# Performance work log

Measured on AMD Instinct MI355X. Metric: run time of the kernel, lower is better.

Reference implementation:

```python
import jax, jax.numpy as jnp
import numpy as np

S, B, I, H, O = 256, 128, 512, 1024, 32


def _lstm_layer(x, w_ih, w_hh, b_ih, b_hh):
    # x: [S, B, Din]; PyTorch gate order: i, f, g, o
    xg = jnp.einsum('sbi,gi->sbg', x, w_ih) + b_ih + b_hh  # [S, B, 4H] precomputed input gates
    Hd = w_hh.shape[1]

    def step(carry, xt):
        h, c = carry
        g = xt + h @ w_hh.T  # [B, 4H]
        i, f, gg, o = jnp.split(g, 4, axis=-1)
        c = jax.nn.sigmoid(f) * c + jax.nn.sigmoid(i) * jnp.tanh(gg)
        h = jax.nn.sigmoid(o) * jnp.tanh(c)
        return (h, c), h

    h0 = jnp.zeros((x.shape[1], Hd), x.dtype)
    (_, _), hs = jax.lax.scan(step, (h0, h0), xg)
    return hs  # [S, B, H]


def setup_inputs() -> dict:
    key = jax.random.key(0)
    ks = jax.random.split(key, 12)
    bound = 1.0 / np.sqrt(H)
    u = lambda k, shape: jax.random.uniform(k, shape, jnp.float32, -bound, bound)
    return {
        'input': jax.random.normal(ks[0], (S, B, I), jnp.float32),
        'w_ih_l0': u(ks[1], (4 * H, I)),
        'w_hh_l0': u(ks[2], (4 * H, H)),
        'b_ih_l0': u(ks[3], (4 * H,)),
        'b_hh_l0': u(ks[4], (4 * H,)),
        'w_ih_l1': u(ks[5], (4 * H, H)),
        'w_hh_l1': u(ks[6], (4 * H, H)),
        'b_ih_l1': u(ks[7], (4 * H,)),
        'b_hh_l1': u(ks[8], (4 * H,)),
        'w_out': u(ks[9], (O, H)),
        'b_out': u(ks[10], (O,)),
    }


def reference(input, w_ih_l0, w_hh_l0, b_ih_l0, b_hh_l0,
              w_ih_l1, w_hh_l1, b_ih_l1, b_hh_l1, w_out, b_out):
    h1 = _lstm_layer(input, w_ih_l0, w_hh_l0, b_ih_l0, b_hh_l0)  # layer 0
    h2 = _lstm_layer(h1, w_ih_l1, w_hh_l1, b_ih_l1, b_hh_l1)    # layer 1
    # original: self.h2o(hidden[4]) -> linear head on timestep index 4
    return h2[4] @ w_out.T + b_out  # [B, O]
```

## Files before the change

kernel.cpp:

```cpp
#include <hip/hip_runtime.h>
#include <hip/hip_bf16.h>
#include <math.h>

#define B_SZ 128
#define I_DIM 512
#define H_DIM 1024
#define O_DIM 32
#define G4 4096
#define NSTEP 5

using short8 = __attribute__((ext_vector_type(8))) short;
using f32x4  = __attribute__((ext_vector_type(4))) float;

__device__ inline unsigned short f2bf(float f) {
    unsigned int u = __float_as_uint(f);
    return (unsigned short)((u + 0x7fffu + ((u >> 16) & 1u)) >> 16);
}
__device__ inline float bf2f(unsigned short h) {
    return __uint_as_float(((unsigned int)h) << 16);
}
__device__ inline float sigf(float x) { return 1.f / (1.f + expf(-x)); }

#define MFMA3(ACC, AH, AL, BH, BL)                                           \
    ACC = __builtin_amdgcn_mfma_f32_16x16x32_bf16(AH, BH, ACC, 0, 0, 0);     \
    ACC = __builtin_amdgcn_mfma_f32_16x16x32_bf16(AH, BL, ACC, 0, 0, 0);     \
    ACC = __builtin_amdgcn_mfma_f32_16x16x32_bf16(AL, BH, ACC, 0, 0, 0);

__global__ __launch_bounds__(256) void init_misc(
    float* __restrict__ c0, float* __restrict__ c1,
    unsigned short* __restrict__ h0hi, unsigned short* __restrict__ h0lo,
    unsigned short* __restrict__ h1hi, unsigned short* __restrict__ h1lo,
    const float* __restrict__ bih0, const float* __restrict__ bhh0,
    const float* __restrict__ bih1, const float* __restrict__ bhh1,
    float* __restrict__ bsum0, float* __restrict__ bsum1)
{
    int i = blockIdx.x * 256 + threadIdx.x;
    if (i < B_SZ * H_DIM) {
        c0[i] = 0.f; c1[i] = 0.f;
        h0hi[i] = 0; h0lo[i] = 0; h1hi[i] = 0; h1lo[i] = 0;
    }
    if (i < G4) {
        bsum0[i] = bih0[i] + bhh0[i];
        bsum1[i] = bih1[i] + bhh1[i];
    }
}

__global__ __launch_bounds__(256) void conv_split(
    const float* __restrict__ s0, const float* __restrict__ s1,
    const float* __restrict__ s2, const float* __restrict__ s3,
    const float* __restrict__ s4,
    unsigned short* __restrict__ h0, unsigned short* __restrict__ l0,
    unsigned short* __restrict__ h1, unsigned short* __restrict__ l1,
    unsigned short* __restrict__ h2, unsigned short* __restrict__ l2,
    unsigned short* __restrict__ h3, unsigned short* __restrict__ l3,
    unsigned short* __restrict__ h4, unsigned short* __restrict__ l4)
{
    const long long E0 = 2097152;
    const long long E1 = E0 + 4194304;
    const long long E2 = E1 + 4194304;
    const long long E3 = E2 + 4194304;
    const long long E4 = E3 + 327680;
    long long i4 = ((long long)blockIdx.x * 256 + threadIdx.x) * 4;
    if (i4 >= E4) return;
    const float* s; unsigned short *hh, *ll; long long base;
    if      (i4 < E0) { s = s0; hh = h0; ll = l0; base = 0;  }
    else if (i4 < E1) { s = s1; hh = h1; ll = l1; base = E0; }
    else if (i4 < E2) { s = s2; hh = h2; ll = l2; base = E1; }
    else if (i4 < E3) { s = s3; hh = h3; ll = l3; base = E2; }
    else              { s = s4; hh = h4; ll = l4; base = E3; }
    long long k = i4 - base;
    float4 v = *(const float4*)(s + k);
    ushort4 hv, lv;
    hv.x = f2bf(v.x); lv.x = f2bf(v.x - bf2f(hv.x));
    hv.y = f2bf(v.y); lv.y = f2bf(v.y - bf2f(hv.y));
    hv.z = f2bf(v.z); lv.z = f2bf(v.z - bf2f(hv.z));
    hv.w = f2bf(v.w); lv.w = f2bf(v.w - bf2f(hv.w));
    *(ushort4*)(hh + k) = hv;
    *(ushort4*)(ll + k) = lv;
}

__global__ __launch_bounds__(256) void gemm_in(
    const unsigned short* __restrict__ xhi, const unsigned short* __restrict__ xlo,
    const unsigned short* __restrict__ whi, const unsigned short* __restrict__ wlo,
    const float* __restrict__ bsum, float* __restrict__ xg)
{
    const int tid = threadIdx.x, lane = tid & 63, wv = tid >> 6;
    const int r = lane & 15, g = lane >> 4;
    const int wm = (wv & 1) * 32, wn = (wv >> 1) * 32;
    const int bm = blockIdx.y * 64, bn = blockIdx.x * 64;
    f32x4 acc[2][2];
    const f32x4 z = {0.f, 0.f, 0.f, 0.f};
    acc[0][0] = z; acc[0][1] = z; acc[1][0] = z; acc[1][1] = z;

    const unsigned short* Ah = xhi + (bm + wm + r) * I_DIM + g * 8;
    const unsigned short* Al = xlo + (bm + wm + r) * I_DIM + g * 8;
    const unsigned short* Bh = whi + (bn + wn + r) * I_DIM + g * 8;
    const unsigned short* Bl = wlo + (bn + wn + r) * I_DIM + g * 8;

    #pragma unroll 4
    for (int k = 0; k < I_DIM; k += 32) {
        short8 a0h = *(const short8*)(Ah + k);
        short8 a0l = *(const short8*)(Al + k);
        short8 a1h = *(const short8*)(Ah + 16 * I_DIM + k);
        short8 a1l = *(const short8*)(Al + 16 * I_DIM + k);
        short8 b0h = *(const short8*)(Bh + k);
        short8 b0l = *(const short8*)(Bl + k);
        short8 b1h = *(const short8*)(Bh + 16 * I_DIM + k);
        short8 b1l = *(const short8*)(Bl + 16 * I_DIM + k);
        MFMA3(acc[0][0], a0h, a0l, b0h, b0l);
        MFMA3(acc[0][1], a0h, a0l, b1h, b1l);
        MFMA3(acc[1][0], a1h, a1l, b0h, b0l);
        MFMA3(acc[1][1], a1h, a1l, b1h, b1l);
    }
    #pragma unroll
    for (int mf = 0; mf < 2; ++mf)
        #pragma unroll
        for (int nf = 0; nf < 2; ++nf)
            #pragma unroll
            for (int j = 0; j < 4; ++j) {
                int row = bm + wm + mf * 16 + g * 4 + j;
                int col = bn + wn + nf * 16 + r;
                xg[row * G4 + col] = acc[mf][nf][j] + bsum[col];
            }
}

template<int LAYER>
__global__ __launch_bounds__(512) void lstm_step(
    const unsigned short* __restrict__ a1hi, const unsigned short* __restrict__ a1lo,
    const unsigned short* __restrict__ w1hi, const unsigned short* __restrict__ w1lo,
    const unsigned short* __restrict__ a2hi, const unsigned short* __restrict__ a2lo,
    const unsigned short* __restrict__ w2hi, const unsigned short* __restrict__ w2lo,
    const float* __restrict__ extra,
    float* __restrict__ cst,
    unsigned short* __restrict__ hohi, unsigned short* __restrict__ holo)
{
    __shared__ float lds_p[8][B_SZ][17];
    const int tid = threadIdx.x, lane = tid & 63, wv = tid >> 6;
    const int r = lane & 15, g = lane >> 4;
    const int jb = blockIdx.x * 4;
    const int q = r >> 2, j4 = r & 3;
    const int wrow = q * H_DIM + jb + j4;

    f32x4 acc[8];
    const f32x4 z = {0.f, 0.f, 0.f, 0.f};
    #pragma unroll
    for (int mf = 0; mf < 8; ++mf) acc[mf] = z;

    if (LAYER == 0) {
        const int kb = wv * 128;
        const unsigned short* Wh = w1hi + (long long)wrow * H_DIM + kb + g * 8;
        const unsigned short* Wl = w1lo + (long long)wrow * H_DIM + kb + g * 8;
        const unsigned short* Ah = a1hi + kb + g * 8;
        const unsigned short* Al = a1lo + kb + g * 8;
        #pragma unroll
        for (int ks = 0; ks < 4; ++ks) {
            short8 bh = *(const short8*)(Wh + ks * 32);
            short8 bl = *(const short8*)(Wl + ks * 32);
            #pragma unroll
            for (int mf = 0; mf < 8; ++mf) {
                int off = (mf * 16 + r) * H_DIM + ks * 32;
                short8 ah = *(const short8*)(Ah + off);
                short8 al = *(const short8*)(Al + off);
                MFMA3(acc[mf], ah, al, bh, bl);
            }
        }
    } else {
        const int kb = (wv & 3) * 256;
        const unsigned short* Wsrc_h = (wv < 4) ? w1hi : w2hi;
        const unsigned short* Wsrc_l = (wv < 4) ? w1lo : w2lo;
        const unsigned short* Asrc_h = (wv < 4) ? a1hi : a2hi;
        const unsigned short* Asrc_l = (wv < 4) ? a1lo : a2lo;
        const unsigned short* Wh = Wsrc_h + (long long)wrow * H_DIM + kb + g * 8;
        const unsigned short* Wl = Wsrc_l + (long long)wrow * H_DIM + kb + g * 8;
        const unsigned short* Ah = Asrc_h + kb + g * 8;
        const unsigned short* Al = Asrc_l + kb + g * 8;
        #pragma unroll
        for (int ks = 0; ks < 8; ++ks) {
            short8 bh = *(const short8*)(Wh + ks * 32);
            short8 bl = *(const short8*)(Wl + ks * 32);
            #pragma unroll
            for (int mf = 0; mf < 8; ++mf) {
                int off = (mf * 16 + r) * H_DIM + ks * 32;
                short8 ah = *(const short8*)(Ah + off);
                short8 al = *(const short8*)(Al + off);
                MFMA3(acc[mf], ah, al, bh, bl);
            }
        }
    }

    #pragma unroll
    for (int mf = 0; mf < 8; ++mf)
        #pragma unroll
        for (int j = 0; j < 4; ++j)
            lds_p[wv][mf * 16 + g * 4 + j][r] = acc[mf][j];
    __syncthreads();

    {
        int b = tid & 127, jj = tid >> 7;
        float gs[4];
        #pragma unroll
        for (int qq = 0; qq < 4; ++qq) {
            int col = qq * 4 + jj;
            float s = 0.f;
            #pragma unroll
            for (int w = 0; w < 8; ++w) s += lds_p[w][b][col];
            s += (LAYER == 0) ? extra[b * G4 + qq * H_DIM + jb + jj]
                              : extra[qq * H_DIM + jb + jj];
            gs[qq] = s;
        }
        int idx = b * H_DIM + jb + jj;
        float cn = sigf(gs[1]) * cst[idx] + sigf(gs[0]) * tanhf(gs[2]);
        cst[idx] = cn;
        float h = sigf(gs[3]) * tanhf(cn);
        unsigned short hh = f2bf(h);
        hohi[idx] = hh;
        holo[idx] = f2bf(h - bf2f(hh));
    }
}

__global__ __launch_bounds__(64) void head_kernel(
    const unsigned short* __restrict__ hhi, const unsigned short* __restrict__ hlo,
    const float* __restrict__ w_out, const float* __restrict__ b_out,
    float* __restrict__ out)
{
    int o = blockIdx.x, b = blockIdx.y, lane = threadIdx.x;
    const unsigned short* hp = hhi + b * H_DIM;
    const unsigned short* lp = hlo + b * H_DIM;
    const float* wp = w_out + o * H_DIM;
    float s = 0.f;
    #pragma unroll
    for (int k = lane; k < H_DIM; k += 64)
        s += (bf2f(hp[k]) + bf2f(lp[k])) * wp[k];
    #pragma unroll
    for (int off = 32; off; off >>= 1) s += __shfl_down(s, off);
    if (lane == 0) out[b * O_DIM + o] = s + b_out[o];
}

extern "C" void kernel_launch(void* const* d_in, const int* in_sizes, int n_in,
                              void* d_out, int out_size, void* d_ws, size_t ws_size,
                              hipStream_t stream)
{
    const float* input   = (const float*)d_in[0];
    const float* w_ih_l0 = (const float*)d_in[1];
    const float* w_hh_l0 = (const float*)d_in[2];
    const float* b_ih_l0 = (const float*)d_in[3];
    const float* b_hh_l0 = (const float*)d_in[4];
    const float* w_ih_l1 = (const float*)d_in[5];
    const float* w_hh_l1 = (const float*)d_in[6];
    const float* b_ih_l1 = (const float*)d_in[7];
    const float* b_hh_l1 = (const float*)d_in[8];
    const float* w_out   = (const float*)d_in[9];
    const float* b_out   = (const float*)d_in[10];
    float* out = (float*)d_out;

    char* base = (char*)d_ws;
    size_t off = 0;
    auto alloc = [&](size_t bytes) { char* p = base + off; off = (off + bytes + 255) & ~(size_t)255; return p; };
    unsigned short* wih0_hi = (unsigned short*)alloc(2097152 * 2);
    unsigned short* wih0_lo = (unsigned short*)alloc(2097152 * 2);
    unsigned short* whh0_hi = (unsigned short*)alloc(4194304 * 2);
    unsigned short* whh0_lo = (unsigned short*)alloc(4194304 * 2);
    unsigned short* wih1_hi = (unsigned short*)alloc(4194304 * 2);
    unsigned short* wih1_lo = (unsigned short*)alloc(4194304 * 2);
    unsigned short* whh1_hi = (unsigned short*)alloc(4194304 * 2);
    unsigned short* whh1_lo = (unsigned short*)alloc(4194304 * 2);
    unsigned short* xhi     = (unsigned short*)alloc(327680 * 2);
    unsigned short* xlo     = (unsigned short*)alloc(327680 * 2);
    float* xg0   = (float*)alloc((size_t)NSTEP * B_SZ * G4 * 4);
    float* bsum0 = (float*)alloc(G4 * 4);
    float* bsum1 = (float*)alloc(G4 * 4);
    float* c0    = (float*)alloc(B_SZ * H_DIM * 4);
    float* c1    = (float*)alloc(B_SZ * H_DIM * 4);
    unsigned short* h0hi[2], *h0lo[2], *h1hi[2], *h1lo[2];
    for (int i = 0; i < 2; ++i) {
        h0hi[i] = (unsigned short*)alloc(B_SZ * H_DIM * 2);
        h0lo[i] = (unsigned short*)alloc(B_SZ * H_DIM * 2);
        h1hi[i] = (unsigned short*)alloc(B_SZ * H_DIM * 2);
        h1lo[i] = (unsigned short*)alloc(B_SZ * H_DIM * 2);
    }

    init_misc<<<(B_SZ * H_DIM + 255) / 256, 256, 0, stream>>>(
        c0, c1, h0hi[0], h0lo[0], h1hi[0], h1lo[0],
        b_ih_l0, b_hh_l0, b_ih_l1, b_hh_l1, bsum0, bsum1);

    conv_split<<<(15007744 / 4 + 255) / 256, 256, 0, stream>>>(
        w_ih_l0, w_hh_l0, w_ih_l1, w_hh_l1, input,
        wih0_hi, wih0_lo, whh0_hi, whh0_lo, wih1_hi, wih1_lo,
        whh1_hi, whh1_lo, xhi, xlo);

    gemm_in<<<dim3(G4 / 64, (NSTEP * B_SZ) / 64), 256, 0, stream>>>(
        xhi, xlo, wih0_hi, wih0_lo, bsum0, xg0);

    for (int t = 0; t < NSTEP; ++t) {
        int in = t & 1, o2 = 1 - in;
        lstm_step<0><<<H_DIM / 4, 512, 0, stream>>>(
            h0hi[in], h0lo[in], whh0_hi, whh0_lo,
            nullptr, nullptr, nullptr, nullptr,
            xg0 + (size_t)t * B_SZ * G4, c0, h0hi[o2], h0lo[o2]);
        lstm_step<1><<<H_DIM / 4, 512, 0, stream>>>(
            h0hi[o2], h0lo[o2], wih1_hi, wih1_lo,
            h1hi[in], h1lo[in], whh1_hi, whh1_lo,
            bsum1, c1, h1hi[o2], h1lo[o2]);
    }

    head_kernel<<<dim3(O_DIM, B_SZ), 64, 0, stream>>>(
        h1hi[1], h1lo[1], w_out, b_out, out);
}
```

Baseline: 519.5 us.

## Pack bf16 weights and hidden states into MFMA fragment-tiled layout

The fp32-to-bf16 hi/lo conversion now writes weights, input and hidden states in a pre-tiled layout where each 16x32 MFMA fragment is contiguous, so every lane loads its short8 from consecutive addresses. The gemm_in, lstm_step and head kernels index this tiled layout, and the recurrent weights are grouped per output block so the gate rows a block needs sit together. The goal is fully coalesced global loads in place of strided row accesses. In exchange the conversion kernel does scattered writes, the hidden-state stores become scattered 2-byte writes, and the cell state is stored transposed.

```diff
diff --git a/kernel.cpp b/kernel.cpp
--- a/kernel.cpp
+++ b/kernel.cpp
@@ -25,6 +25,7 @@
     ACC = __builtin_amdgcn_mfma_f32_16x16x32_bf16(AH, BH, ACC, 0, 0, 0);     \
     ACC = __builtin_amdgcn_mfma_f32_16x16x32_bf16(AH, BL, ACC, 0, 0, 0);     \
     ACC = __builtin_amdgcn_mfma_f32_16x16x32_bf16(AL, BH, ACC, 0, 0, 0);
+
 
 __global__ __launch_bounds__(256) void init_misc(
     float* __restrict__ c0, float* __restrict__ c1,
@@ -45,68 +46,85 @@
     }
 }
 
-__global__ __launch_bounds__(256) void conv_split(
-    const float* __restrict__ s0, const float* __restrict__ s1,
-    const float* __restrict__ s2, const float* __restrict__ s3,
-    const float* __restrict__ s4,
-    unsigned short* __restrict__ h0, unsigned short* __restrict__ l0,
-    unsigned short* __restrict__ h1, unsigned short* __restrict__ l1,
-    unsigned short* __restrict__ h2, unsigned short* __restrict__ l2,
-    unsigned short* __restrict__ h3, unsigned short* __restrict__ l3,
-    unsigned short* __restrict__ h4, unsigned short* __restrict__ l4)
-{
-    const long long E0 = 2097152;
-    const long long E1 = E0 + 4194304;
-    const long long E2 = E1 + 4194304;
-    const long long E3 = E2 + 4194304;
-    const long long E4 = E3 + 327680;
-    long long i4 = ((long long)blockIdx.x * 256 + threadIdx.x) * 4;
-    if (i4 >= E4) return;
-    const float* s; unsigned short *hh, *ll; long long base;
-    if      (i4 < E0) { s = s0; hh = h0; ll = l0; base = 0;  }
-    else if (i4 < E1) { s = s1; hh = h1; ll = l1; base = E0; }
-    else if (i4 < E2) { s = s2; hh = h2; ll = l2; base = E1; }
-    else if (i4 < E3) { s = s3; hh = h3; ll = l3; base = E2; }
-    else              { s = s4; hh = h4; ll = l4; base = E3; }
-    long long k = i4 - base;
-    float4 v = *(const float4*)(s + k);
-    ushort4 hv, lv;
-    hv.x = f2bf(v.x); lv.x = f2bf(v.x - bf2f(hv.x));
-    hv.y = f2bf(v.y); lv.y = f2bf(v.y - bf2f(hv.y));
-    hv.z = f2bf(v.z); lv.z = f2bf(v.z - bf2f(hv.z));
-    hv.w = f2bf(v.w); lv.w = f2bf(v.w - bf2f(hv.w));
-    *(ushort4*)(hh + k) = hv;
-    *(ushort4*)(ll + k) = lv;
+__global__ __launch_bounds__(256) void conv_pack(
+    const float* __restrict__ s_wih0, const float* __restrict__ s_whh0,
+    const float* __restrict__ s_wih1, const float* __restrict__ s_whh1,
+    const float* __restrict__ s_x,
+    unsigned short* __restrict__ d_wih0h, unsigned short* __restrict__ d_wih0l,
+    unsigned short* __restrict__ d_whh0h, unsigned short* __restrict__ d_whh0l,
+    unsigned short* __restrict__ d_wih1h, unsigned short* __restrict__ d_wih1l,
+    unsigned short* __restrict__ d_whh1h, unsigned short* __restrict__ d_whh1l,
+    unsigned short* __restrict__ d_xh,   unsigned short* __restrict__ d_xl)
+{
+    const long long G0 = 262144;
+    const long long G1 = G0 + 524288;
+    const long long G2 = G1 + 524288;
+    const long long G3 = G2 + 524288;
+    const long long GT = G3 + 40960;
+    long long i8 = (long long)blockIdx.x * 256 + threadIdx.x;
+    if (i8 >= GT) return;
+    const float* src; unsigned short *dh, *dl;
+    int row, k8, K, blockpk;
+    if (i8 < G0)      { long long lg = i8;      src = s_wih0; dh = d_wih0h; dl = d_wih0l; K = 512;  blockpk = 0; row = (int)(lg >> 6);  k8 = (int)(lg & 63);  }
+    else if (i8 < G1) { long long lg = i8 - G0; src = s_whh0; dh = d_whh0h; dl = d_whh0l; K = 1024; blockpk = 1; row = (int)(lg >> 7);  k8 = (int)(lg & 127); }
+    else if (i8 < G2) { long long lg = i8 - G1; src = s_wih1; dh = d_wih1h; dl = d_wih1l; K = 1024; blockpk = 1; row = (int)(lg >> 7);  k8 = (int)(lg & 127); }
+    else if (i8 < G3) { long long lg = i8 - G2; src = s_whh1; dh = d_whh1h; dl = d_whh1l; K = 1024; blockpk = 1; row = (int)(lg >> 7);  k8 = (int)(lg & 127); }
+    else              { long long lg = i8 - G3; src = s_x;    dh = d_xh;    dl = d_xl;    K = 512;  blockpk = 0; row = (int)(lg >> 6);  k8 = (int)(lg & 63);  }
+    int kt = k8 >> 2, g = k8 & 3;
+    long long dst;
+    if (blockpk) {
+        int j = row & 1023, q = row >> 10;
+        int r = q * 4 + (j & 3);
+        dst = (((long long)(j >> 2) * 32 + kt) * 64 + g * 16 + r) * 8;
+    } else {
+        int NKT = K >> 5;
+        dst = (((long long)(row >> 4) * NKT + kt) * 64 + g * 16 + (row & 15)) * 8;
+    }
+    const float* p = src + (long long)row * K + k8 * 8;
+    float4 a = *(const float4*)p;
+    float4 b = *(const float4*)(p + 4);
+    float v[8] = {a.x, a.y, a.z, a.w, b.x, b.y, b.z, b.w};
+    short8 hv, lv;
+    #pragma unroll
+    for (int i = 0; i < 8; ++i) {
+        unsigned short h = f2bf(v[i]);
+        hv[i] = (short)h;
+        lv[i] = (short)f2bf(v[i] - bf2f(h));
+    }
+    *(short8*)(dh + dst) = hv;
+    *(short8*)(dl + dst) = lv;
 }
 
 __global__ __launch_bounds__(256) void gemm_in(
-    const unsigned short* __restrict__ xhi, const unsigned short* __restrict__ xlo,
-    const unsigned short* __restrict__ whi, const unsigned short* __restrict__ wlo,
+    const unsigned short* __restrict__ xh, const unsigned short* __restrict__ xl,
+    const unsigned short* __restrict__ wh, const unsigned short* __restrict__ wl,
     const float* __restrict__ bsum, float* __restrict__ xg)
 {
     const int tid = threadIdx.x, lane = tid & 63, wv = tid >> 6;
     const int r = lane & 15, g = lane >> 4;
     const int wm = (wv & 1) * 32, wn = (wv >> 1) * 32;
     const int bm = blockIdx.y * 64, bn = blockIdx.x * 64;
+    const int art = (bm + wm) >> 4, brt = (bn + wn) >> 4;
     f32x4 acc[2][2];
     const f32x4 z = {0.f, 0.f, 0.f, 0.f};
     acc[0][0] = z; acc[0][1] = z; acc[1][0] = z; acc[1][1] = z;
 
-    const unsigned short* Ah = xhi + (bm + wm + r) * I_DIM + g * 8;
-    const unsigned short* Al = xlo + (bm + wm + r) * I_DIM + g * 8;
-    const unsigned short* Bh = whi + (bn + wn + r) * I_DIM + g * 8;
-    const unsigned short* Bl = wlo + (bn + wn + r) * I_DIM + g * 8;
+    const unsigned short* A0h = xh + (long long)art * 8192 + lane * 8;
+    const unsigned short* A0l = xl + (long long)art * 8192 + lane * 8;
+    const unsigned short* B0h = wh + (long long)brt * 8192 + lane * 8;
+    const unsigned short* B0l = wl + (long long)brt * 8192 + lane * 8;
 
     #pragma unroll 4
-    for (int k = 0; k < I_DIM; k += 32) {
-        short8 a0h = *(const short8*)(Ah + k);
-        short8 a0l = *(const short8*)(Al + k);
-        short8 a1h = *(const short8*)(Ah + 16 * I_DIM + k);
-        short8 a1l = *(const short8*)(Al + 16 * I_DIM + k);
-        short8 b0h = *(const short8*)(Bh + k);
-        short8 b0l = *(const short8*)(Bl + k);
-        short8 b1h = *(const short8*)(Bh + 16 * I_DIM + k);
-        short8 b1l = *(const short8*)(Bl + 16 * I_DIM + k);
+    for (int kt = 0; kt < 16; ++kt) {
+        int o = kt * 512;
+        short8 a0h = *(const short8*)(A0h + o);
+        short8 a0l = *(const short8*)(A0l + o);
+        short8 a1h = *(const short8*)(A0h + 8192 + o);
+        short8 a1l = *(const short8*)(A0l + 8192 + o);
+        short8 b0h = *(const short8*)(B0h + o);
+        short8 b0l = *(const short8*)(B0l + o);
+        short8 b1h = *(const short8*)(B0h + 8192 + o);
+        short8 b1l = *(const short8*)(B0l + 8192 + o);
         MFMA3(acc[0][0], a0h, a0l, b0h, b0l);
         MFMA3(acc[0][1], a0h, a0l, b1h, b1l);
         MFMA3(acc[1][0], a1h, a1l, b0h, b0l);
@@ -120,7 +138,7 @@
             for (int j = 0; j < 4; ++j) {
                 int row = bm + wm + mf * 16 + g * 4 + j;
                 int col = bn + wn + nf * 16 + r;
-                xg[row * G4 + col] = acc[mf][nf][j] + bsum[col];
+                xg[(long long)row * G4 + col] = acc[mf][nf][j] + bsum[col];
             }
 }
 
@@ -138,8 +156,6 @@
     const int tid = threadIdx.x, lane = tid & 63, wv = tid >> 6;
     const int r = lane & 15, g = lane >> 4;
     const int jb = blockIdx.x * 4;
-    const int q = r >> 2, j4 = r & 3;
-    const int wrow = q * H_DIM + jb + j4;
 
     f32x4 acc[8];
     const f32x4 z = {0.f, 0.f, 0.f, 0.f};
@@ -147,42 +163,40 @@
     for (int mf = 0; mf < 8; ++mf) acc[mf] = z;
 
     if (LAYER == 0) {
-        const int kb = wv * 128;
-        const unsigned short* Wh = w1hi + (long long)wrow * H_DIM + kb + g * 8;
-        const unsigned short* Wl = w1lo + (long long)wrow * H_DIM + kb + g * 8;
-        const unsigned short* Ah = a1hi + kb + g * 8;
-        const unsigned short* Al = a1lo + kb + g * 8;
+        const unsigned short* Wh = w1hi + (long long)blockIdx.x * 16384 + lane * 8;
+        const unsigned short* Wl = w1lo + (long long)blockIdx.x * 16384 + lane * 8;
+        const unsigned short* Ah = a1hi + lane * 8;
+        const unsigned short* Al = a1lo + lane * 8;
+        const int kt0 = wv * 4;
         #pragma unroll
         for (int ks = 0; ks < 4; ++ks) {
-            short8 bh = *(const short8*)(Wh + ks * 32);
-            short8 bl = *(const short8*)(Wl + ks * 32);
+            const int kt = kt0 + ks;
+            short8 bh = *(const short8*)(Wh + kt * 512);
+            short8 bl = *(const short8*)(Wl + kt * 512);
             #pragma unroll
             for (int mf = 0; mf < 8; ++mf) {
-                int off = (mf * 16 + r) * H_DIM + ks * 32;
-                short8 ah = *(const short8*)(Ah + off);
-                short8 al = *(const short8*)(Al + off);
+                long long o = ((long long)mf * 32 + kt) * 512;
+                short8 ah = *(const short8*)(Ah + o);
+                short8 al = *(const short8*)(Al + o);
                 MFMA3(acc[mf], ah, al, bh, bl);
             }
         }
     } else {
-        const int kb = (wv & 3) * 256;
-        const unsigned short* Wsrc_h = (wv < 4) ? w1hi : w2hi;
-        const unsigned short* Wsrc_l = (wv < 4) ? w1lo : w2lo;
-        const unsigned short* Asrc_h = (wv < 4) ? a1hi : a2hi;
-        const unsigned short* Asrc_l = (wv < 4) ? a1lo : a2lo;
-        const unsigned short* Wh = Wsrc_h + (long long)wrow * H_DIM + kb + g * 8;
-        const unsigned short* Wl = Wsrc_l + (long long)wrow * H_DIM + kb + g * 8;
-        const unsigned short* Ah = Asrc_h + kb + g * 8;
-        const unsigned short* Al = Asrc_l + kb + g * 8;
+        const unsigned short* Wh = ((wv < 4) ? w1hi : w2hi) + (long long)blockIdx.x * 16384 + lane * 8;
+        const unsigned short* Wl = ((wv < 4) ? w1lo : w2lo) + (long long)blockIdx.x * 16384 + lane * 8;
+        const unsigned short* Ah = ((wv < 4) ? a1hi : a2hi) + lane * 8;
+        const unsigned short* Al = ((wv < 4) ? a1lo : a2lo) + lane * 8;
+        const int kt0 = (wv & 3) * 8;
         #pragma unroll
         for (int ks = 0; ks < 8; ++ks) {
-            short8 bh = *(const short8*)(Wh + ks * 32);
-            short8 bl = *(const short8*)(Wl + ks * 32);
+            const int kt = kt0 + ks;
+            short8 bh = *(const short8*)(Wh + kt * 512);
+            short8 bl = *(const short8*)(Wl + kt * 512);
             #pragma unroll
             for (int mf = 0; mf < 8; ++mf) {
-                int off = (mf * 16 + r) * H_DIM + ks * 32;
-                short8 ah = *(const short8*)(Ah + off);
-                short8 al = *(const short8*)(Al + off);
+                long long o = ((long long)mf * 32 + kt) * 512;
+                short8 ah = *(const short8*)(Ah + o);
+                short8 al = *(const short8*)(Al + o);
                 MFMA3(acc[mf], ah, al, bh, bl);
             }
         }
@@ -196,25 +210,28 @@
     __syncthreads();
 
     {
-        int b = tid & 127, jj = tid >> 7;
+        const int b = tid & 127, jj = tid >> 7;
+        const int jout = jb + jj;
         float gs[4];
         #pragma unroll
         for (int qq = 0; qq < 4; ++qq) {
-            int col = qq * 4 + jj;
+            const int col = qq * 4 + jj;
             float s = 0.f;
             #pragma unroll
             for (int w = 0; w < 8; ++w) s += lds_p[w][b][col];
-            s += (LAYER == 0) ? extra[b * G4 + qq * H_DIM + jb + jj]
-                              : extra[qq * H_DIM + jb + jj];
+            s += (LAYER == 0) ? extra[(long long)b * G4 + qq * H_DIM + jout]
+                              : extra[qq * H_DIM + jout];
             gs[qq] = s;
         }
-        int idx = b * H_DIM + jb + jj;
-        float cn = sigf(gs[1]) * cst[idx] + sigf(gs[0]) * tanhf(gs[2]);
-        cst[idx] = cn;
+        const int cidx = jout * B_SZ + b;
+        float cn = sigf(gs[1]) * cst[cidx] + sigf(gs[0]) * tanhf(gs[2]);
+        cst[cidx] = cn;
         float h = sigf(gs[3]) * tanhf(cn);
+        const long long di = (((long long)(b >> 4) * 32 + (jout >> 5)) * 64
+                              + ((jout >> 3) & 3) * 16 + (b & 15)) * 8 + (jout & 7);
         unsigned short hh = f2bf(h);
-        hohi[idx] = hh;
-        holo[idx] = f2bf(h - bf2f(hh));
+        hohi[di] = hh;
+        holo[di] = f2bf(h - bf2f(hh));
     }
 }
 
@@ -224,13 +241,14 @@
     float* __restrict__ out)
 {
     int o = blockIdx.x, b = blockIdx.y, lane = threadIdx.x;
-    const unsigned short* hp = hhi + b * H_DIM;
-    const unsigned short* lp = hlo + b * H_DIM;
-    const float* wp = w_out + o * H_DIM;
+    const float* wp = w_out + (long long)o * H_DIM;
+    const long long rb = (long long)(b >> 4) * 32;
+    const int rr = b & 15;
     float s = 0.f;
-    #pragma unroll
-    for (int k = lane; k < H_DIM; k += 64)
-        s += (bf2f(hp[k]) + bf2f(lp[k])) * wp[k];
+    for (int k = lane; k < H_DIM; k += 64) {
+        long long di = ((rb + (k >> 5)) * 64 + ((k >> 3) & 3) * 16 + rr) * 8 + (k & 7);
+        s += (bf2f(hhi[di]) + bf2f(hlo[di])) * wp[k];
+    }
     #pragma unroll
     for (int off = 32; off; off >>= 1) s += __shfl_down(s, off);
     if (lane == 0) out[b * O_DIM + o] = s + b_out[o];
@@ -283,7 +301,7 @@
         c0, c1, h0hi[0], h0lo[0], h1hi[0], h1lo[0],
         b_ih_l0, b_hh_l0, b_ih_l1, b_hh_l1, bsum0, bsum1);
 
-    conv_split<<<(15007744 / 4 + 255) / 256, 256, 0, stream>>>(
+    conv_pack<<<7328, 256, 0, stream>>>(
         w_ih_l0, w_hh_l0, w_ih_l1, w_hh_l1, input,
         wih0_hi, wih0_lo, whh0_hi, whh0_lo, wih1_hi, wih1_lo,
         whh1_hi, whh1_lo, xhi, xlo);
```

Result: faster. 417.5 us (-19.6%).
